# Kernel tuning notes

Hardware: AMD Instinct MI355X
Metric: run time of the kernel (lower is better)

## Reference

```python
import jax, jax.numpy as jnp
import numpy as np

N_NODES = 50000
N_EDGES = 500000
IN_CH = 128
OUT_CH = 128
N_TYPES = 2
NEG_SLOPE = 0.2
EPS = 1e-16


def setup_inputs() -> dict:
    key = jax.random.key(0)
    ks = jax.random.split(key, 8)
    x = jax.random.normal(ks[0], (N_NODES, IN_CH), dtype=jnp.float32)
    edge_index = jax.random.randint(ks[1], (2, N_EDGES), 0, N_NODES, dtype=jnp.int64)
    edge_type = jax.random.randint(ks[2], (N_EDGES,), 0, N_TYPES, dtype=jnp.int64)
    # xavier-uniform-like params
    def xav(k, shape, fan_in, fan_out):
        lim = np.sqrt(6.0 / (fan_in + fan_out)).astype(np.float32)
        return jax.random.uniform(k, shape, jnp.float32, -lim, lim)
    weight = xav(ks[3], (N_TYPES, IN_CH, OUT_CH), IN_CH, OUT_CH)
    att = xav(ks[4], (N_TYPES, 2 * OUT_CH), N_TYPES, 2 * OUT_CH)
    root_w = xav(ks[5], (OUT_CH, IN_CH), IN_CH, OUT_CH)
    lim = 1.0 / np.sqrt(IN_CH)
    root_b = jax.random.uniform(ks[6], (OUT_CH,), jnp.float32, -lim, lim)
    return {"x": x, "edge_index": edge_index, "edge_type": edge_type,
            "weight": weight, "att": att, "root_w": root_w, "root_b": root_b}


def reference(x, edge_index, edge_type, weight, att, root_w, root_b):
    n = x.shape[0]
    src, dst = edge_index[0], edge_index[1]
    # Per-edge transform x[src] @ W[edge_type] == gather from per-type node transforms
    h_all = jnp.einsum('ni,tio->nto', x, weight)          # [N, T, O]
    h_src = h_all[src, edge_type]                          # [E, O]
    h_dst = h_all[dst, edge_type]                          # [E, O]
    a = att[edge_type]                                     # [E, 2O]
    o = h_src.shape[1]
    e = (h_src * a[:, :o]).sum(-1) + (h_dst * a[:, o:]).sum(-1)
    e = jnp.where(e > 0, e, NEG_SLOPE * e)                 # leaky_relu
    # segment softmax over dst (stable: subtract per-segment max)
    seg_max = jax.ops.segment_max(e, dst, num_segments=n)
    ex = jnp.exp(e - seg_max[dst])
    denom = jax.ops.segment_sum(ex, dst, num_segments=n)
    alpha = ex / (denom[dst] + EPS)
    # dropout is identity in eval mode
    msg = h_src * alpha[:, None]
    out = jax.ops.segment_sum(msg, dst, num_segments=n)
    out = out + x @ root_w.T + root_b
    return out
```

## Files before the change

kernel.cpp:

```cpp
#include <hip/hip_runtime.h>
#include <hip/hip_bf16.h>

#define N_NODES 50000
#define N_EDGES 500000
#define IN_CH 128
#define OUT_CH 128
#define N_TYPES 2
#define NEG_SLOPE 0.2f
#define EPS_F 1e-16f

typedef __attribute__((ext_vector_type(8))) short bf16x8;
typedef __attribute__((ext_vector_type(4))) float f32x4;

__device__ __forceinline__ unsigned short bf16_rne(float f) {
    unsigned int u = __float_as_uint(f);
    u += 0x7FFFu + ((u >> 16) & 1u);
    return (unsigned short)(u >> 16);
}
__device__ __forceinline__ float bf16_to_f32(unsigned short h) {
    return __uint_as_float(((unsigned int)h) << 16);
}

__global__ __launch_bounds__(256) void bprep_kernel(
    const float* __restrict__ weight, const float* __restrict__ root_w,
    unsigned short* __restrict__ bt_hi, unsigned short* __restrict__ bt_lo)
{
    int i = blockIdx.x * 256 + threadIdx.x;
    if (i >= 384 * 128) return;
    int n = i >> 7, k = i & 127;
    float v;
    if (n < 256) {
        int t = n >> 7, o = n & 127;
        v = weight[(size_t)t * 16384 + (size_t)k * 128 + o];
    } else {
        v = root_w[(size_t)(n - 256) * 128 + k];
    }
    unsigned short h = bf16_rne(v);
    float lo = v - bf16_to_f32(h);
    bt_hi[i] = h;
    bt_lo[i] = bf16_rne(lo);
}

#define MBLK 391
#define LSWZ(row, col) ((row) * 128 + ((col) ^ (((row) & 7) << 3)))

__global__ __launch_bounds__(256) void mfma_gemm_kernel(
    const float* __restrict__ x,
    const unsigned short* __restrict__ bt_hi,
    const unsigned short* __restrict__ bt_lo,
    const float* __restrict__ root_b,
    float* __restrict__ hall, float* __restrict__ out)
{
    __shared__ unsigned short Ah[128 * 128];
    __shared__ unsigned short Al[128 * 128];
    __shared__ unsigned short Bh[128 * 128];
    __shared__ unsigned short Bl[128 * 128];

    const int tid = threadIdx.x;
    const int bid = blockIdx.x;
    const int c = bid / MBLK;
    const int m0 = (bid - c * MBLK) * 128;

    {
        const float4* xg = (const float4*)x;
        #pragma unroll
        for (int it = 0; it < 16; ++it) {
            int idx = tid + it * 256;
            int r = idx >> 5, c4 = idx & 31;
            int gn = m0 + r;
            float4 v = make_float4(0.f, 0.f, 0.f, 0.f);
            if (gn < N_NODES) v = xg[(size_t)gn * 32 + c4];
            unsigned short h0 = bf16_rne(v.x), h1 = bf16_rne(v.y),
                           h2 = bf16_rne(v.z), h3 = bf16_rne(v.w);
            ushort4 hh = make_ushort4(h0, h1, h2, h3);
            ushort4 ll = make_ushort4(bf16_rne(v.x - bf16_to_f32(h0)),
                                      bf16_rne(v.y - bf16_to_f32(h1)),
                                      bf16_rne(v.z - bf16_to_f32(h2)),
                                      bf16_rne(v.w - bf16_to_f32(h3)));
            int off = LSWZ(r, c4 * 4);
            *(ushort4*)&Ah[off] = hh;
            *(ushort4*)&Al[off] = ll;
        }
    }

    {
        const float4* bhg = (const float4*)(bt_hi + (size_t)c * 128 * 128);
        const float4* blg = (const float4*)(bt_lo + (size_t)c * 128 * 128);
        #pragma unroll
        for (int it = 0; it < 8; ++it) {
            int f4 = tid + it * 256;
            int r = f4 >> 4, c8 = f4 & 15;
            int off = LSWZ(r, c8 * 8);
            *(float4*)&Bh[off] = bhg[f4];
            *(float4*)&Bl[off] = blg[f4];
        }
    }
    __syncthreads();

    const int lane = tid & 63;
    const int w = tid >> 6;
    const int mh = (w >> 1) * 64;
    const int nh = (w & 1) * 64;
    const int lr = lane & 15;
    const int lk = (lane >> 4) * 8;

    f32x4 acc[4][4];
    #pragma unroll
    for (int mi = 0; mi < 4; ++mi)
        #pragma unroll
        for (int ni = 0; ni < 4; ++ni)
            acc[mi][ni] = (f32x4){0.f, 0.f, 0.f, 0.f};

    #pragma unroll
    for (int ks = 0; ks < 4; ++ks) {
        const int ko = ks * 32 + lk;
        bf16x8 ah[4], al[4], bh[4], bl[4];
        #pragma unroll
        for (int mi = 0; mi < 4; ++mi) {
            int off = LSWZ(mh + mi * 16 + lr, ko);
            ah[mi] = *(const bf16x8*)&Ah[off];
            al[mi] = *(const bf16x8*)&Al[off];
        }
        #pragma unroll
        for (int ni = 0; ni < 4; ++ni) {
            int off = LSWZ(nh + ni * 16 + lr, ko);
            bh[ni] = *(const bf16x8*)&Bh[off];
            bl[ni] = *(const bf16x8*)&Bl[off];
        }
        #pragma unroll
        for (int mi = 0; mi < 4; ++mi)
            #pragma unroll
            for (int ni = 0; ni < 4; ++ni) {
                acc[mi][ni] = __builtin_amdgcn_mfma_f32_16x16x32_bf16(
                    ah[mi], bh[ni], acc[mi][ni], 0, 0, 0);
                acc[mi][ni] = __builtin_amdgcn_mfma_f32_16x16x32_bf16(
                    ah[mi], bl[ni], acc[mi][ni], 0, 0, 0);
                acc[mi][ni] = __builtin_amdgcn_mfma_f32_16x16x32_bf16(
                    al[mi], bh[ni], acc[mi][ni], 0, 0, 0);
            }
    }

    const int crow = (lane >> 4) * 4;
    const int ccol = lane & 15;
    if (c < 2) {
        #pragma unroll
        for (int mi = 0; mi < 4; ++mi)
            #pragma unroll
            for (int j = 0; j < 4; ++j) {
                int gm = m0 + mh + mi * 16 + crow + j;
                if (gm < N_NODES) {
                    #pragma unroll
                    for (int ni = 0; ni < 4; ++ni) {
                        int n = nh + ni * 16 + ccol;
                        hall[((size_t)gm * 2 + c) * 128 + n] = acc[mi][ni][j];
                    }
                }
            }
    } else {
        float rbv[4];
        #pragma unroll
        for (int ni = 0; ni < 4; ++ni) rbv[ni] = root_b[nh + ni * 16 + ccol];
        #pragma unroll
        for (int mi = 0; mi < 4; ++mi)
            #pragma unroll
            for (int j = 0; j < 4; ++j) {
                int gm = m0 + mh + mi * 16 + crow + j;
                if (gm < N_NODES) {
                    #pragma unroll
                    for (int ni = 0; ni < 4; ++ni) {
                        int n = nh + ni * 16 + ccol;
                        out[(size_t)gm * 128 + n] = acc[mi][ni][j] + rbv[ni];
                    }
                }
            }
    }
}

__global__ __launch_bounds__(256) void hist_kernel(
    const int* __restrict__ ei, int* __restrict__ deg)
{
    int i = blockIdx.x * 256 + threadIdx.x;
    if (i < N_EDGES) atomicAdd(&deg[ei[N_EDGES + i]], 1);
}

__global__ __launch_bounds__(256) void scan1_kernel(
    const int* __restrict__ deg, int* __restrict__ rp, int* __restrict__ bsum)
{
    __shared__ int s[256];
    int i = blockIdx.x * 256 + threadIdx.x;
    int v = (i < N_NODES) ? deg[i] : 0;
    s[threadIdx.x] = v;
    __syncthreads();
    #pragma unroll
    for (int off = 1; off < 256; off <<= 1) {
        int t = (threadIdx.x >= off) ? s[threadIdx.x - off] : 0;
        __syncthreads();
        s[threadIdx.x] += t;
        __syncthreads();
    }
    if (i < N_NODES) rp[i + 1] = s[threadIdx.x];
    if (threadIdx.x == 255) bsum[blockIdx.x] = s[255];
    if (i == 0) rp[0] = 0;
}

__global__ __launch_bounds__(256) void scan2_kernel(int* __restrict__ bsum, int nb)
{
    __shared__ int s[256];
    int tid = threadIdx.x;
    int v = (tid < nb) ? bsum[tid] : 0;
    s[tid] = v;
    __syncthreads();
    #pragma unroll
    for (int off = 1; off < 256; off <<= 1) {
        int t = (tid >= off) ? s[tid - off] : 0;
        __syncthreads();
        s[tid] += t;
        __syncthreads();
    }
    if (tid < nb) bsum[tid] = s[tid] - v;
}

__global__ __launch_bounds__(256) void scan3_kernel(
    int* __restrict__ rp, const int* __restrict__ bsum)
{
    int i = blockIdx.x * 256 + threadIdx.x;
    if (i < N_NODES) rp[i + 1] += bsum[blockIdx.x];
}

__global__ __launch_bounds__(256) void csr_scatter_kernel(
    const int* __restrict__ ei, const int* __restrict__ etype,
    const int* __restrict__ rp, int* __restrict__ cursor, int* __restrict__ skey)
{
    int i = blockIdx.x * 256 + threadIdx.x;
    if (i >= N_EDGES) return;
    int dst = ei[N_EDGES + i];
    int pos = rp[dst] + atomicAdd(&cursor[dst], 1);
    skey[pos] = (ei[i] << 1) | (etype[i] & 1);
}

__global__ __launch_bounds__(256) void node_agg_kernel(
    const int* __restrict__ rp, const int* __restrict__ skey,
    const float* __restrict__ hall, const float* __restrict__ att,
    float* __restrict__ out)
{
    const int lane = threadIdx.x & 63;
    const int node = (blockIdx.x * 256 + threadIdx.x) >> 6;
    if (node >= N_NODES) return;
    const int row0 = rp[node], row1 = rp[node + 1];
    if (row0 == row1) return;

    const float2 al0 = *(const float2*)&att[0 * 256 + lane * 2];
    const float2 ar0 = *(const float2*)&att[0 * 256 + 128 + lane * 2];
    const float2 al1 = *(const float2*)&att[1 * 256 + lane * 2];
    const float2 ar1 = *(const float2*)&att[1 * 256 + 128 + lane * 2];

    const float2 hd0 = *(const float2*)&hall[((size_t)node * 2 + 0) * 128 + lane * 2];
    const float2 hd1 = *(const float2*)&hall[((size_t)node * 2 + 1) * 128 + lane * 2];
    float dr0 = hd0.x * ar0.x + hd0.y * ar0.y;
    float dr1 = hd1.x * ar1.x + hd1.y * ar1.y;
    #pragma unroll
    for (int off = 32; off; off >>= 1) {
        dr0 += __shfl_xor(dr0, off);
        dr1 += __shfl_xor(dr1, off);
    }

    const float NINF = -__builtin_inff();
    float m = NINF, denom = 0.f, a0 = 0.f, a1 = 0.f;

    for (int j = row0; j < row1; j += 4) {
        const int je = row1 - 1;
        const int k0 = skey[j];
        const int k1 = skey[min(j + 1, je)];
        const int k2 = skey[min(j + 2, je)];
        const int k3 = skey[min(j + 3, je)];
        const int t0 = k0 & 1, t1 = k1 & 1, t2 = k2 & 1, t3 = k3 & 1;

        const float2 h0 = *(const float2*)&hall[((size_t)(k0 >> 1) * 2 + t0) * 128 + lane * 2];
        const float2 h1 = *(const float2*)&hall[((size_t)(k1 >> 1) * 2 + t1) * 128 + lane * 2];
        const float2 h2 = *(const float2*)&hall[((size_t)(k2 >> 1) * 2 + t2) * 128 + lane * 2];
        const float2 h3 = *(const float2*)&hall[((size_t)(k3 >> 1) * 2 + t3) * 128 + lane * 2];

        const float2 A0 = t0 ? al1 : al0;
        const float2 A1 = t1 ? al1 : al0;
        const float2 A2 = t2 ? al1 : al0;
        const float2 A3 = t3 ? al1 : al0;

        float p0 = h0.x * A0.x + h0.y * A0.y;
        float p1 = h1.x * A1.x + h1.y * A1.y;
        float p2 = h2.x * A2.x + h2.y * A2.y;
        float p3 = h3.x * A3.x + h3.y * A3.y;
        #pragma unroll
        for (int off = 32; off; off >>= 1) {
            p0 += __shfl_xor(p0, off);
            p1 += __shfl_xor(p1, off);
            p2 += __shfl_xor(p2, off);
            p3 += __shfl_xor(p3, off);
        }

        float e0 = p0 + (t0 ? dr1 : dr0);
        float e1 = p1 + (t1 ? dr1 : dr0);
        float e2 = p2 + (t2 ? dr1 : dr0);
        float e3 = p3 + (t3 ? dr1 : dr0);
        e0 = (e0 > 0.f) ? e0 : NEG_SLOPE * e0;
        e1 = (e1 > 0.f) ? e1 : NEG_SLOPE * e1;
        e2 = (e2 > 0.f) ? e2 : NEG_SLOPE * e2;
        e3 = (e3 > 0.f) ? e3 : NEG_SLOPE * e3;
        if (j + 1 > je) e1 = NINF;
        if (j + 2 > je) e2 = NINF;
        if (j + 3 > je) e3 = NINF;

        const float mx = fmaxf(fmaxf(fmaxf(e0, e1), fmaxf(e2, e3)), m);
        if (mx > m) {
            const float r = __expf(m - mx);
            denom *= r; a0 *= r; a1 *= r;
            m = mx;
        }
        const float w0 = __expf(e0 - m);
        const float w1 = __expf(e1 - m);
        const float w2 = __expf(e2 - m);
        const float w3 = __expf(e3 - m);
        denom += (w0 + w1) + (w2 + w3);
        a0 += w0 * h0.x + w1 * h1.x + w2 * h2.x + w3 * h3.x;
        a1 += w0 * h0.y + w1 * h1.y + w2 * h2.y + w3 * h3.y;
    }
    const float inv = 1.f / (denom + EPS_F);
    float* op = &out[(size_t)node * 128 + lane * 2];
    op[0] += a0 * inv;
    op[1] += a1 * inv;
}

extern "C" void kernel_launch(void* const* d_in, const int* in_sizes, int n_in,
                              void* d_out, int out_size, void* d_ws, size_t ws_size,
                              hipStream_t stream) {
    const float* x      = (const float*)d_in[0];
    const int*   ei     = (const int*)d_in[1];
    const int*   etype  = (const int*)d_in[2];
    const float* weight = (const float*)d_in[3];
    const float* att    = (const float*)d_in[4];
    const float* root_w = (const float*)d_in[5];
    const float* root_b = (const float*)d_in[6];
    float* out = (float*)d_out;

    float* hall  = (float*)d_ws;
    int* deg     = (int*)(hall + (size_t)N_NODES * 2 * 128);
    int* cursor  = deg + N_NODES;
    int* rp      = cursor + N_NODES;
    int* bsum    = rp + (N_NODES + 1);
    int* skey    = bsum + 256;
    unsigned short* bt_hi = (unsigned short*)(skey + N_EDGES);
    unsigned short* bt_lo = bt_hi + 384 * 128;

    const int NB_E = (N_EDGES + 255) / 256;
    const int NB_N = (N_NODES + 255) / 256;

    hipMemsetAsync(deg, 0, sizeof(int) * (size_t)N_NODES * 2, stream);

    bprep_kernel<<<192, 256, 0, stream>>>(weight, root_w, bt_hi, bt_lo);

    mfma_gemm_kernel<<<3 * MBLK, 256, 0, stream>>>(
        x, bt_hi, bt_lo, root_b, hall, out);

    hist_kernel<<<NB_E, 256, 0, stream>>>(ei, deg);
    scan1_kernel<<<NB_N, 256, 0, stream>>>(deg, rp, bsum);
    scan2_kernel<<<1, 256, 0, stream>>>(bsum, NB_N);
    scan3_kernel<<<NB_N, 256, 0, stream>>>(rp, bsum);
    csr_scatter_kernel<<<NB_E, 256, 0, stream>>>(ei, etype, rp, cursor, skey);

    node_agg_kernel<<<(N_NODES + 3) / 4, 256, 0, stream>>>(
        rp, skey, hall, att, out);
}
```

Baseline: 249.8 us.

## Process two nodes per wavefront in aggregation and read GEMM B operand from global

The aggregation kernel now assigns 32 lanes per destination node with float4 loads, so each wavefront handles two nodes and the shuffle reductions are one step shorter. The online softmax rescale becomes branchless. Separately, the GEMM kernel drops its LDS staging of the B operand and loads B fragments straight from global memory, halving LDS use so it can declare two blocks per CU. The risks are lane divergence when the two nodes in a wavefront have different degrees, and higher global/L2 traffic for B fragments in the GEMM.

```diff
diff --git a/kernel.cpp b/kernel.cpp
--- a/kernel.cpp
+++ b/kernel.cpp
@@ -44,7 +44,7 @@
 #define MBLK 391
 #define LSWZ(row, col) ((row) * 128 + ((col) ^ (((row) & 7) << 3)))
 
-__global__ __launch_bounds__(256) void mfma_gemm_kernel(
+__global__ __launch_bounds__(256, 2) void mfma_gemm_kernel(
     const float* __restrict__ x,
     const unsigned short* __restrict__ bt_hi,
     const unsigned short* __restrict__ bt_lo,
@@ -53,8 +53,6 @@
 {
     __shared__ unsigned short Ah[128 * 128];
     __shared__ unsigned short Al[128 * 128];
-    __shared__ unsigned short Bh[128 * 128];
-    __shared__ unsigned short Bl[128 * 128];
 
     const int tid = threadIdx.x;
     const int bid = blockIdx.x;
@@ -82,19 +80,6 @@
             *(ushort4*)&Al[off] = ll;
         }
     }
-
-    {
-        const float4* bhg = (const float4*)(bt_hi + (size_t)c * 128 * 128);
-        const float4* blg = (const float4*)(bt_lo + (size_t)c * 128 * 128);
-        #pragma unroll
-        for (int it = 0; it < 8; ++it) {
-            int f4 = tid + it * 256;
-            int r = f4 >> 4, c8 = f4 & 15;
-            int off = LSWZ(r, c8 * 8);
-            *(float4*)&Bh[off] = bhg[f4];
-            *(float4*)&Bl[off] = blg[f4];
-        }
-    }
     __syncthreads();
 
     const int lane = tid & 63;
@@ -104,6 +89,11 @@
     const int lr = lane & 15;
     const int lk = (lane >> 4) * 8;
 
+    const unsigned short* bh_base =
+        bt_hi + ((size_t)(c * 128 + nh + lr)) * 128 + lk;
+    const unsigned short* bl_base =
+        bt_lo + ((size_t)(c * 128 + nh + lr)) * 128 + lk;
+
     f32x4 acc[4][4];
     #pragma unroll
     for (int mi = 0; mi < 4; ++mi)
@@ -114,18 +104,18 @@
     #pragma unroll
     for (int ks = 0; ks < 4; ++ks) {
         const int ko = ks * 32 + lk;
-        bf16x8 ah[4], al[4], bh[4], bl[4];
+        bf16x8 bh[4], bl[4];
+        #pragma unroll
+        for (int ni = 0; ni < 4; ++ni) {
+            bh[ni] = *(const bf16x8*)(bh_base + ni * 2048 + ks * 32);
+            bl[ni] = *(const bf16x8*)(bl_base + ni * 2048 + ks * 32);
+        }
+        bf16x8 ah[4], al[4];
         #pragma unroll
         for (int mi = 0; mi < 4; ++mi) {
             int off = LSWZ(mh + mi * 16 + lr, ko);
             ah[mi] = *(const bf16x8*)&Ah[off];
             al[mi] = *(const bf16x8*)&Al[off];
-        }
-        #pragma unroll
-        for (int ni = 0; ni < 4; ++ni) {
-            int off = LSWZ(nh + ni * 16 + lr, ko);
-            bh[ni] = *(const bf16x8*)&Bh[off];
-            bl[ni] = *(const bf16x8*)&Bl[off];
         }
         #pragma unroll
         for (int mi = 0; mi < 4; ++mi)
@@ -238,34 +228,41 @@
     skey[pos] = (ei[i] << 1) | (etype[i] & 1);
 }
 
+__device__ __forceinline__ float dot4(float4 a, float4 b) {
+    return a.x * b.x + a.y * b.y + a.z * b.z + a.w * b.w;
+}
+
 __global__ __launch_bounds__(256) void node_agg_kernel(
     const int* __restrict__ rp, const int* __restrict__ skey,
     const float* __restrict__ hall, const float* __restrict__ att,
     float* __restrict__ out)
 {
     const int lane = threadIdx.x & 63;
-    const int node = (blockIdx.x * 256 + threadIdx.x) >> 6;
+    const int sl = lane & 31;
+    const int half = lane >> 5;
+    const int wid = (blockIdx.x * 256 + threadIdx.x) >> 6;
+    const int node = wid * 2 + half;
     if (node >= N_NODES) return;
     const int row0 = rp[node], row1 = rp[node + 1];
-    if (row0 == row1) return;
-
-    const float2 al0 = *(const float2*)&att[0 * 256 + lane * 2];
-    const float2 ar0 = *(const float2*)&att[0 * 256 + 128 + lane * 2];
-    const float2 al1 = *(const float2*)&att[1 * 256 + lane * 2];
-    const float2 ar1 = *(const float2*)&att[1 * 256 + 128 + lane * 2];
-
-    const float2 hd0 = *(const float2*)&hall[((size_t)node * 2 + 0) * 128 + lane * 2];
-    const float2 hd1 = *(const float2*)&hall[((size_t)node * 2 + 1) * 128 + lane * 2];
-    float dr0 = hd0.x * ar0.x + hd0.y * ar0.y;
-    float dr1 = hd1.x * ar1.x + hd1.y * ar1.y;
-    #pragma unroll
-    for (int off = 32; off; off >>= 1) {
+
+    const float4 al0 = *(const float4*)&att[0 * 256 + sl * 4];
+    const float4 ar0 = *(const float4*)&att[0 * 256 + 128 + sl * 4];
+    const float4 al1 = *(const float4*)&att[1 * 256 + sl * 4];
+    const float4 ar1 = *(const float4*)&att[1 * 256 + 128 + sl * 4];
+
+    const float4 hd0 = *(const float4*)&hall[((size_t)node * 2 + 0) * 128 + sl * 4];
+    const float4 hd1 = *(const float4*)&hall[((size_t)node * 2 + 1) * 128 + sl * 4];
+    float dr0 = dot4(hd0, ar0);
+    float dr1 = dot4(hd1, ar1);
+    #pragma unroll
+    for (int off = 16; off; off >>= 1) {
         dr0 += __shfl_xor(dr0, off);
         dr1 += __shfl_xor(dr1, off);
     }
 
     const float NINF = -__builtin_inff();
-    float m = NINF, denom = 0.f, a0 = 0.f, a1 = 0.f;
+    float m = NINF, denom = 0.f;
+    float4 acc = make_float4(0.f, 0.f, 0.f, 0.f);
 
     for (int j = row0; j < row1; j += 4) {
         const int je = row1 - 1;
@@ -275,22 +272,17 @@
         const int k3 = skey[min(j + 3, je)];
         const int t0 = k0 & 1, t1 = k1 & 1, t2 = k2 & 1, t3 = k3 & 1;
 
-        const float2 h0 = *(const float2*)&hall[((size_t)(k0 >> 1) * 2 + t0) * 128 + lane * 2];
-        const float2 h1 = *(const float2*)&hall[((size_t)(k1 >> 1) * 2 + t1) * 128 + lane * 2];
-        const float2 h2 = *(const float2*)&hall[((size_t)(k2 >> 1) * 2 + t2) * 128 + lane * 2];
-        const float2 h3 = *(const float2*)&hall[((size_t)(k3 >> 1) * 2 + t3) * 128 + lane * 2];
-
-        const float2 A0 = t0 ? al1 : al0;
-        const float2 A1 = t1 ? al1 : al0;
-        const float2 A2 = t2 ? al1 : al0;
-        const float2 A3 = t3 ? al1 : al0;
-
-        float p0 = h0.x * A0.x + h0.y * A0.y;
-        float p1 = h1.x * A1.x + h1.y * A1.y;
-        float p2 = h2.x * A2.x + h2.y * A2.y;
-        float p3 = h3.x * A3.x + h3.y * A3.y;
-        #pragma unroll
-        for (int off = 32; off; off >>= 1) {
+        const float4 h0 = *(const float4*)&hall[((size_t)(k0 >> 1) * 2 + t0) * 128 + sl * 4];
+        const float4 h1 = *(const float4*)&hall[((size_t)(k1 >> 1) * 2 + t1) * 128 + sl * 4];
+        const float4 h2 = *(const float4*)&hall[((size_t)(k2 >> 1) * 2 + t2) * 128 + sl * 4];
+        const float4 h3 = *(const float4*)&hall[((size_t)(k3 >> 1) * 2 + t3) * 128 + sl * 4];
+
+        float p0 = dot4(h0, t0 ? al1 : al0);
+        float p1 = dot4(h1, t1 ? al1 : al0);
+        float p2 = dot4(h2, t2 ? al1 : al0);
+        float p3 = dot4(h3, t3 ? al1 : al0);
+        #pragma unroll
+        for (int off = 16; off; off >>= 1) {
             p0 += __shfl_xor(p0, off);
             p1 += __shfl_xor(p1, off);
             p2 += __shfl_xor(p2, off);
@@ -309,24 +301,31 @@
         if (j + 2 > je) e2 = NINF;
         if (j + 3 > je) e3 = NINF;
 
-        const float mx = fmaxf(fmaxf(fmaxf(e0, e1), fmaxf(e2, e3)), m);
-        if (mx > m) {
-            const float r = __expf(m - mx);
-            denom *= r; a0 *= r; a1 *= r;
-            m = mx;
-        }
+        const float mx = fmaxf(fmaxf(e0, e1), fmaxf(e2, e3));
+        const float mn = fmaxf(m, mx);
+        const float r = __expf(m - mn);
+        m = mn;
         const float w0 = __expf(e0 - m);
         const float w1 = __expf(e1 - m);
         const float w2 = __expf(e2 - m);
         const float w3 = __expf(e3 - m);
-        denom += (w0 + w1) + (w2 + w3);
-        a0 += w0 * h0.x + w1 * h1.x + w2 * h2.x + w3 * h3.x;
-        a1 += w0 * h0.y + w1 * h1.y + w2 * h2.y + w3 * h3.y;
-    }
-    const float inv = 1.f / (denom + EPS_F);
-    float* op = &out[(size_t)node * 128 + lane * 2];
-    op[0] += a0 * inv;
-    op[1] += a1 * inv;
+        denom = denom * r + (w0 + w1) + (w2 + w3);
+        acc.x = acc.x * r + w0 * h0.x + w1 * h1.x + w2 * h2.x + w3 * h3.x;
+        acc.y = acc.y * r + w0 * h0.y + w1 * h1.y + w2 * h2.y + w3 * h3.y;
+        acc.z = acc.z * r + w0 * h0.z + w1 * h1.z + w2 * h2.z + w3 * h3.z;
+        acc.w = acc.w * r + w0 * h0.w + w1 * h1.w + w2 * h2.w + w3 * h3.w;
+    }
+
+    if (row0 < row1) {
+        const float inv = 1.f / (denom + EPS_F);
+        float4* op = (float4*)&out[(size_t)node * 128 + sl * 4];
+        float4 o = *op;
+        o.x += acc.x * inv;
+        o.y += acc.y * inv;
+        o.z += acc.z * inv;
+        o.w += acc.w * inv;
+        *op = o;
+    }
 }
 
 extern "C" void kernel_launch(void* const* d_in, const int* in_sizes, int n_in,
@@ -366,6 +365,6 @@
     scan3_kernel<<<NB_N, 256, 0, stream>>>(rp, bsum);
     csr_scatter_kernel<<<NB_E, 256, 0, stream>>>(ei, etype, rp, cursor, skey);
 
-    node_agg_kernel<<<(N_NODES + 3) / 4, 256, 0, stream>>>(
+    node_agg_kernel<<<(N_NODES + 7) / 8, 256, 0, stream>>>(
         rp, skey, hall, att, out);
 }
```

Result: faster. 240.8 us (-3.6%).
